# Kernel optimization log

Measured on AMD Instinct MI355X. Metric: run time of the kernel, lower is better.

Reference implementation:

```python
import jax, jax.numpy as jnp
import numpy as np

B, N, D, H, M, O = 8, 1024, 256, 512, 256, 256


def _mlp(x, W1, b1, W2, b2):
    # two-layer MLP: Linear -> ReLU -> Linear (torch Linear: x @ W.T + b)
    return jax.nn.relu(x @ W1.T + b1) @ W2.T + b2


def _lstm(x, W_ih, W_hh, b):
    # x: [B, N, D] -> h: [B, N, H]; single-layer unidirectional LSTM, torch gate order i,f,g,o
    Bt, Nt, _ = x.shape
    x_proj = x @ W_ih.T + b  # [B, N, 4H] precompute input projection

    def step(carry, xt):
        h, c = carry
        gates = xt + h @ W_hh.T
        i, f, g, o = jnp.split(gates, 4, axis=-1)
        i, f, o = jax.nn.sigmoid(i), jax.nn.sigmoid(f), jax.nn.sigmoid(o)
        c = f * c + i * jnp.tanh(g)
        h = o * jnp.tanh(c)
        return (h, c), h

    h0 = jnp.zeros((Bt, W_hh.shape[1]), x.dtype)
    (_, _), hs = jax.lax.scan(step, (h0, h0), jnp.swapaxes(x_proj, 0, 1))
    return jnp.swapaxes(hs, 0, 1)


def setup_inputs() -> dict:
    key = jax.random.key(0)
    ks = jax.random.split(key, 32)
    p = lambda k, s: jax.random.normal(k, s, jnp.float32) * 0.02
    inp = {
        "feats": jax.random.normal(ks[0], (B, N, D), jnp.float32),
        "adj": jax.random.randint(ks[1], (B, N, N), 0, 2, jnp.int32),
        "W_ih": p(ks[2], (4 * H, D)),
        "W_hh": p(ks[3], (4 * H, H)),
        "b_ih": jnp.zeros((4 * H,), jnp.float32),
        "b_hh": jnp.zeros((4 * H,), jnp.float32),
        "gx_W1": p(ks[4], (M, H)), "gx_b1": jnp.zeros((M,), jnp.float32),
        "gx_W2": p(ks[5], (M, M)), "gx_b2": jnp.zeros((M,), jnp.float32),
        "gz_W1": p(ks[6], (M, H)), "gz_b1": jnp.zeros((M,), jnp.float32),
        "gz_W2": p(ks[7], (M, M)), "gz_b2": jnp.zeros((M,), jnp.float32),
        "gv_W1": p(ks[8], (M, H)), "gv_b1": jnp.zeros((M,), jnp.float32),
        "gv_W2": p(ks[9], (M, M)), "gv_b2": jnp.zeros((M,), jnp.float32),
        "gn_W1": p(ks[10], (M, M)), "gn_b1": jnp.zeros((M,), jnp.float32),
        "gn_W2": p(ks[11], (O, M)), "gn_b2": jnp.zeros((O,), jnp.float32),
        "out_W": p(ks[12], (O, H + O)), "out_b": jnp.zeros((O,), jnp.float32),
    }
    return inp


def reference(feats, adj, W_ih, W_hh, b_ih, b_hh,
              gx_W1, gx_b1, gx_W2, gx_b2,
              gz_W1, gz_b1, gz_W2, gz_b2,
              gv_W1, gv_b1, gv_W2, gv_b2,
              gn_W1, gn_b1, gn_W2, gn_b2,
              out_W, out_b):
    h = _lstm(feats, W_ih, W_hh, b_ih + b_hh)  # [B, N, H]

    # Note: in the source, concat_1[:, :lstm_hidden_dim] == s_i and
    # concat_2[:, :lstm_hidden_dim] == s_j, so scores = <g_x(s_i), g_v(s_j)>
    ax = _mlp(h, gx_W1, gx_b1, gx_W2, gx_b2)  # [B, N, M]
    av = _mlp(h, gv_W1, gv_b1, gv_W2, gv_b2)  # [B, N, M]
    scores = jnp.einsum('bim,bjm->bij', ax, av)  # [B, N, N]

    eye = jnp.eye(N, dtype=bool)
    mask = (adj > 0) & ~eye[None]  # valid neighbors
    w = jax.nn.softmax(jnp.where(mask, scores, -1e30), axis=-1)
    w = w * mask  # zero out rows with no neighbors (softmax of all -inf -> uniform)

    sagg = jnp.einsum('bij,bjh->bih', w, h)  # weighted neighbor sum [B, N, H]
    agg = _mlp(_mlp(sagg, gz_W1, gz_b1, gz_W2, gz_b2), gn_W1, gn_b1, gn_W2, gn_b2)
    has_nb = mask.any(axis=-1, keepdims=True)  # [B, N, 1]
    agg = jnp.where(has_nb, agg, 0.0)  # isolated nodes get zero aggregate

    combined = jnp.concatenate([h, agg], axis=-1)  # [B, N, H+O]
    return combined @ out_W.T + out_b
```

## Files before the change

### kernel.cpp

```cpp
#include <hip/hip_runtime.h>

typedef unsigned short u16;
typedef unsigned long long u64;
using short8 = __attribute__((ext_vector_type(8))) short;
using f32x4  = __attribute__((ext_vector_type(4))) float;

#define GF_RELU  1
#define GF_F32   2
#define GF_XPOSE 4

__device__ __forceinline__ float b2f(u16 x) {
    unsigned u = ((unsigned)x) << 16;
    return __builtin_bit_cast(float, u);
}
__device__ __forceinline__ u16 f2b(float f) {
    unsigned u = __builtin_bit_cast(unsigned, f);
    unsigned r = u + 0x7FFFu + ((u >> 16) & 1u);
    return (u16)(r >> 16);
}
__device__ __forceinline__ f32x4 mfma_bf16(uint4 a, uint4 b, f32x4 c) {
    return __builtin_amdgcn_mfma_f32_16x16x32_bf16(
        __builtin_bit_cast(short8, a), __builtin_bit_cast(short8, b), c, 0, 0, 0);
}
__device__ __forceinline__ f32x4 zero4() { f32x4 z = {0.f, 0.f, 0.f, 0.f}; return z; }

__global__ __launch_bounds__(256) void cvt_bf16(const float* __restrict__ src,
                                                u16* __restrict__ dst, int n) {
    for (int i = blockIdx.x * 256 + threadIdx.x; i < n; i += gridDim.x * 256)
        dst[i] = f2b(src[i]);
}

__global__ void pack_params(const float* __restrict__ Whh, const float* __restrict__ Wih,
                            const float* __restrict__ bih, const float* __restrict__ bhh,
                            u16* __restrict__ WhhP, u16* __restrict__ WihP,
                            float* __restrict__ biasP) {
    int p = blockIdx.x;
    int t = threadIdx.x;
    int orig = ((p & 3) << 9) + (p >> 2);
    WhhP[((long)p << 9) + t]       = f2b(Whh[((long)orig << 9) + t]);
    WhhP[((long)p << 9) + 256 + t] = f2b(Whh[((long)orig << 9) + 256 + t]);
    WihP[((long)p << 8) + t]       = f2b(Wih[((long)orig << 8) + t]);
    if (t == 0) biasP[p] = bih[orig] + bhh[orig];
}

__global__ __launch_bounds__(256) void gemm_bt(
    const u16* __restrict__ A, const u16* __restrict__ A2, int ksplit,
    const u16* __restrict__ B, void* __restrict__ Cout,
    int M, int N, int K,
    long sAb, long sBb, long sCb,
    const float* __restrict__ bias, const float* __restrict__ rowmask, int flags) {
    __shared__ __align__(16) u16 As[64][40];
    __shared__ __align__(16) u16 Bs[128][40];
    const int bz = blockIdx.z;
    const u16* Ab = A + (long)bz * sAb;
    const u16* Bb = B + (long)bz * sBb;
    const int m0 = blockIdx.x << 6, n0 = blockIdx.y << 7;
    const int tid = threadIdx.x;
    const int lane = tid & 63, wave = tid >> 6;
    const int srow = tid >> 2, skc = (tid & 3) << 3;
    const int frm = lane & 15, fq = lane >> 4;

    auto loadA = [&](int ka) -> uint4 {
        const u16* p = (ka < ksplit)
            ? Ab + (long)(m0 + srow) * ksplit + ka
            : A2 + (long)(m0 + srow) * (K - ksplit) + (ka - ksplit);
        return *(const uint4*)p;
    };
    const u16* Brow0 = Bb + (long)(n0 + srow) * K;
    const u16* Brow1 = Bb + (long)(n0 + 64 + srow) * K;

    f32x4 acc[8];
#pragma unroll
    for (int i = 0; i < 8; i++) acc[i] = zero4();

    uint4 a  = loadA(skc);
    uint4 b0 = *(const uint4*)(Brow0 + skc);
    uint4 b1 = *(const uint4*)(Brow1 + skc);

    for (int k0 = 0; k0 < K; k0 += 32) {
        __syncthreads();
        *(uint4*)&As[srow][skc] = a;
        *(uint4*)&Bs[srow][skc] = b0;
        *(uint4*)&Bs[64 + srow][skc] = b1;
        __syncthreads();
        int kn = k0 + 32;
        if (kn < K) {
            a  = loadA(kn + skc);
            b0 = *(const uint4*)(Brow0 + kn + skc);
            b1 = *(const uint4*)(Brow1 + kn + skc);
        }
        uint4 af = *(const uint4*)&As[(wave << 4) + frm][fq << 3];
#pragma unroll
        for (int nt = 0; nt < 8; nt++) {
            uint4 bf = *(const uint4*)&Bs[(nt << 4) + frm][fq << 3];
            acc[nt] = mfma_bf16(af, bf, acc[nt]);
        }
    }
#pragma unroll
    for (int nt = 0; nt < 8; nt++) {
        int col = n0 + (nt << 4) + frm;
        float bv = bias ? bias[col] : 0.f;
#pragma unroll
        for (int r = 0; r < 4; r++) {
            int row = m0 + (wave << 4) + (fq << 2) + r;
            float v = acc[nt][r] + bv;
            if (flags & GF_RELU) v = fmaxf(v, 0.f);
            if (rowmask) v *= rowmask[row];
            long orow = (flags & GF_XPOSE) ? (long)((row & 1023) * 8 + (row >> 10))
                                           : (long)row;
            if (flags & GF_F32)
                ((float*)Cout)[(long)bz * sCb + orow * N + col] = v;
            else
                ((u16*)Cout)[(long)bz * sCb + orow * N + col] = f2b(v);
        }
    }
}

template<bool L2C>
__device__ __forceinline__ void lstm_loop(
    const u16* __restrict__ xproj, u16* __restrict__ h, u64* __restrict__ hx,
    const uint4 (&bfrag)[2][16], unsigned* hsh, int* hflag,
    int g, int s, int wv, int lane, int frm, int fq, int colbase) {
    float creg = 0.f;
    int budget = 1 << 20;

#pragma unroll 1
    for (int t = 0; t < 1024; t++) {
        float xp0 = b2f(xproj[((long)(t * 8 + g) << 11) + colbase + frm]);
        float xp1 = b2f(xproj[((long)(t * 8 + g) << 11) + colbase + 16 + frm]);

        float s0, s1;
        if (t > 0) {
            if (wv == 0) {
                const u64* buf = hx + (g << 9) + (((t - 1) & 1) << 8);
                const u64* p0 = buf + lane;
                const u64* p1 = buf + 64 + lane;
                const u64* p2 = buf + 128 + lane;
                const u64* p3 = buf + 192 + lane;
                u64 v0, v1, v2, v3;
                const unsigned want = (unsigned)t;
                while (true) {
                    if constexpr (L2C) {
                        u64 z = 0;
                        asm volatile(
                            "global_atomic_add_x2 %0, %4, %8, off sc0\n\t"
                            "global_atomic_add_x2 %1, %5, %8, off sc0\n\t"
                            "global_atomic_add_x2 %2, %6, %8, off sc0\n\t"
                            "global_atomic_add_x2 %3, %7, %8, off sc0\n\t"
                            "s_waitcnt vmcnt(0)"
                            : "=&v"(v0), "=&v"(v1), "=&v"(v2), "=&v"(v3)
                            : "v"(p0), "v"(p1), "v"(p2), "v"(p3), "v"(z)
                            : "memory");
                    } else {
                        asm volatile(
                            "global_load_dwordx2 %0, %4, off sc0 sc1\n\t"
                            "global_load_dwordx2 %1, %5, off sc0 sc1\n\t"
                            "global_load_dwordx2 %2, %6, off sc0 sc1\n\t"
                            "global_load_dwordx2 %3, %7, off sc0 sc1\n\t"
                            "s_waitcnt vmcnt(0)"
                            : "=&v"(v0), "=&v"(v1), "=&v"(v2), "=&v"(v3)
                            : "v"(p0), "v"(p1), "v"(p2), "v"(p3)
                            : "memory");
                    }
                    bool ok = ((unsigned)(v0 >> 32) == want) &
                              ((unsigned)(v1 >> 32) == want) &
                              ((unsigned)(v2 >> 32) == want) &
                              ((unsigned)(v3 >> 32) == want);
                    if (__all(ok) || --budget < 0) break;
                }
                hsh[lane]       = (unsigned)v0;
                hsh[64 + lane]  = (unsigned)v1;
                hsh[128 + lane] = (unsigned)v2;
                hsh[192 + lane] = (unsigned)v3;
                __threadfence_block();
                if (lane == 0)
                    __hip_atomic_store(hflag, t, __ATOMIC_RELAXED,
                                       __HIP_MEMORY_SCOPE_WORKGROUP);
            } else {
                while (__hip_atomic_load(hflag, __ATOMIC_RELAXED,
                                         __HIP_MEMORY_SCOPE_WORKGROUP) < t) {
                    if (--budget < 0) break;
                }
                __threadfence_block();
            }

            f32x4 a0p[4], a1p[4];
#pragma unroll
            for (int r = 0; r < 4; r++) { a0p[r] = zero4(); a1p[r] = zero4(); }
#pragma unroll
            for (int r4 = 0; r4 < 4; r4++) {
                uint4 af[4];
#pragma unroll
                for (int q = 0; q < 4; q++)
                    af[q] = *(const uint4*)&hsh[(((r4 << 2) | q) << 4) + (fq << 2)];
#pragma unroll
                for (int q = 0; q < 4; q++) {
                    a0p[r4] = mfma_bf16(af[q], bfrag[0][(r4 << 2) | q], a0p[r4]);
                    a1p[r4] = mfma_bf16(af[q], bfrag[1][(r4 << 2) | q], a1p[r4]);
                }
            }
            s0 = (a0p[0][0] + a0p[1][0]) + (a0p[2][0] + a0p[3][0]) + xp0;
            s1 = (a1p[0][0] + a1p[1][0]) + (a1p[2][0] + a1p[3][0]) + xp1;
        } else {
            s0 = xp0;
            s1 = xp1;
        }

        float ss[4];
#pragma unroll
        for (int k = 0; k < 4; k++) {
            int src = ((lane << 2) + k) & 15;
            float t0 = __shfl(s0, src);
            float t1 = __shfl(s1, src);
            ss[k] = (lane < 4) ? t0 : t1;
        }
        float iv = 1.f / (1.f + __expf(-ss[0]));
        float fv = 1.f / (1.f + __expf(-ss[1]));
        float gv = 1.f - 2.f / (__expf(2.f * ss[2]) + 1.f);
        float ov = 1.f / (1.f + __expf(-ss[3]));
        creg = fv * creg + iv * gv;
        float hv = ov * (1.f - 2.f / (__expf(2.f * creg) + 1.f));
        float hn = __shfl_down(hv, 1);
        if (lane < 8 && !(lane & 1)) {
            unsigned dw = (unsigned)f2b(hv) | ((unsigned)f2b(hn) << 16);
            int d = (s << 5) + (wv << 2) + (lane >> 1);
            u64 pv = ((u64)(unsigned)(t + 1) << 32) | (u64)dw;
            u64* dst = &hx[(g << 9) + ((t & 1) << 8) + d];
            if constexpr (L2C) {
                asm volatile("global_atomic_swap_x2 %0, %1, off"
                             :: "v"(dst), "v"(pv) : "memory");
            } else {
                asm volatile("global_store_dwordx2 %0, %1, off sc0 sc1"
                             :: "v"(dst), "v"(pv) : "memory");
            }
            ((unsigned*)h)[(((long)(g * 1024 + t)) << 8) + d] = dw;
        }
    }
}

__global__ __launch_bounds__(512, 1) void lstm_rec(
    const u16* __restrict__ WhhP, const u16* __restrict__ xproj,
    u16* __restrict__ h, u64* __restrict__ hx, unsigned* __restrict__ xcdid) {
    __shared__ __align__(16) unsigned hshare[256];
    __shared__ int hflag;
    const int bid = blockIdx.x;
    const int g = bid & 7;
    const int s = bid >> 3;
    const int tid = threadIdx.x;
    const int lane = tid & 63, wv = tid >> 6;
    const int frm = lane & 15, fq = lane >> 4;
    const int colbase = (s << 8) + (wv << 5);

    uint4 bfrag[2][16];
#pragma unroll
    for (int T = 0; T < 2; T++)
#pragma unroll
        for (int kk = 0; kk < 16; kk++)
            bfrag[T][kk] = *(const uint4*)&WhhP[((long)(colbase + (T << 4) + frm) << 9) +
                                                (kk << 5) + (fq << 3)];

    unsigned myxcd;
    asm volatile("s_getreg_b32 %0, hwreg(HW_REG_XCC_ID)" : "=s"(myxcd));
    if (tid == 0) {
        hflag = -1;
        unsigned val = 0x100u | (myxcd & 0xffu);
        asm volatile("global_store_dword %0, %1, off sc0 sc1"
                     :: "v"(&xcdid[bid]), "v"(val) : "memory");
    }
    const unsigned* pid = &xcdid[g + ((lane & 7) << 3)];
    unsigned idv = 0;
    int bd = 1 << 22;
    while (true) {
        asm volatile("global_load_dword %0, %1, off sc0 sc1\n\ts_waitcnt vmcnt(0)"
                     : "=&v"(idv) : "v"(pid) : "memory");
        if (__all((idv >> 8) == 1u) || --bd < 0) break;
    }
    bool same = (bd >= 0) && __all((idv & 0xffu) == (__shfl(idv, 0) & 0xffu));
    __syncthreads();

    if (same)
        lstm_loop<true>(xproj, h, hx, bfrag, hshare, &hflag,
                        g, s, wv, lane, frm, fq, colbase);
    else
        lstm_loop<false>(xproj, h, hx, bfrag, hshare, &hflag,
                         g, s, wv, lane, frm, fq, colbase);
}

__global__ __launch_bounds__(256) void transpose_h(const u16* __restrict__ h,
                                                   u16* __restrict__ hT) {
    __shared__ __align__(16) u16 tile[64][72];
    const int b = blockIdx.z;
    const int t0 = blockIdx.x << 6, u0 = blockIdx.y << 6;
    const int tid = threadIdx.x;
    const int r = tid >> 3, c8 = (tid & 7) << 3;
#pragma unroll
    for (int j = 0; j < 2; j++) {
        int row = r + (j << 5);
        *(uint4*)&tile[row][c8] =
            *(const uint4*)&h[(((long)b << 10) + t0 + row) * 512 + u0 + c8];
    }
    __syncthreads();
#pragma unroll
    for (int j = 0; j < 2; j++) {
        int urow = r + (j << 5);
        unsigned wds[4];
#pragma unroll
        for (int k = 0; k < 4; k++) {
            unsigned lo = tile[c8 + (k << 1)][urow];
            unsigned hi = tile[c8 + (k << 1) + 1][urow];
            wds[k] = lo | (hi << 16);
        }
        uint4 v; v.x = wds[0]; v.y = wds[1]; v.z = wds[2]; v.w = wds[3];
        *(uint4*)&hT[(((long)b << 9) + u0 + urow) * 1024 + t0 + c8] = v;
    }
}

__global__ __launch_bounds__(256) void softmax_row(
    const float* __restrict__ scores, const int* __restrict__ adj,
    u16* __restrict__ w, float* __restrict__ hasnb) {
    __shared__ float red[4];
    const int row = blockIdx.x;
    const int i = row & 1023;
    const int tid = threadIdx.x;
    const int lane = tid & 63, wave = tid >> 6;
    const float* s = scores + ((long)row << 10);
    const int* arow = adj + ((long)row << 10);

    float sv[4]; bool mk[4];
    float mx = -3.0e38f;
#pragma unroll
    for (int q = 0; q < 4; q++) {
        int j = tid + (q << 8);
        mk[q] = (arow[j] > 0) && (j != i);
        sv[q] = s[j];
        if (mk[q]) mx = fmaxf(mx, sv[q]);
    }
    for (int off = 32; off; off >>= 1) mx = fmaxf(mx, __shfl_xor(mx, off));
    if (lane == 0) red[wave] = mx;
    __syncthreads();
    mx = fmaxf(fmaxf(red[0], red[1]), fmaxf(red[2], red[3]));
    float e[4]; float sum = 0.f;
#pragma unroll
    for (int q = 0; q < 4; q++) {
        e[q] = mk[q] ? __expf(sv[q] - mx) : 0.f;
        sum += e[q];
    }
    __syncthreads();
    for (int off = 32; off; off >>= 1) sum += __shfl_xor(sum, off);
    if (lane == 0) red[wave] = sum;
    __syncthreads();
    sum = red[0] + red[1] + red[2] + red[3];
    float inv = sum > 0.f ? 1.f / sum : 0.f;
#pragma unroll
    for (int q = 0; q < 4; q++) {
        int j = tid + (q << 8);
        w[((long)row << 10) + j] = f2b(e[q] * inv);
    }
    if (tid == 0) hasnb[row] = sum > 0.f ? 1.f : 0.f;
}

extern "C" void kernel_launch(void* const* d_in, const int* in_sizes, int n_in,
                              void* d_out, int out_size, void* d_ws, size_t ws_size,
                              hipStream_t stream) {
    const float* feats = (const float*)d_in[0];
    const int*   adj   = (const int*)d_in[1];
    const float* W_ih  = (const float*)d_in[2];
    const float* W_hh  = (const float*)d_in[3];
    const float* b_ih  = (const float*)d_in[4];
    const float* b_hh  = (const float*)d_in[5];
    const float* gx_W1 = (const float*)d_in[6];  const float* gx_b1 = (const float*)d_in[7];
    const float* gx_W2 = (const float*)d_in[8];  const float* gx_b2 = (const float*)d_in[9];
    const float* gz_W1 = (const float*)d_in[10]; const float* gz_b1 = (const float*)d_in[11];
    const float* gz_W2 = (const float*)d_in[12]; const float* gz_b2 = (const float*)d_in[13];
    const float* gv_W1 = (const float*)d_in[14]; const float* gv_b1 = (const float*)d_in[15];
    const float* gv_W2 = (const float*)d_in[16]; const float* gv_b2 = (const float*)d_in[17];
    const float* gn_W1 = (const float*)d_in[18]; const float* gn_b1 = (const float*)d_in[19];
    const float* gn_W2 = (const float*)d_in[20]; const float* gn_b2 = (const float*)d_in[21];
    const float* out_W = (const float*)d_in[22]; const float* out_b = (const float*)d_in[23];

    char* ws = (char*)d_ws;
    size_t off = 0;
    auto alloc = [&](size_t bytes) {
        void* p = ws + off;
        off += (bytes + 255) & ~(size_t)255;
        return p;
    };
    u16* WhhP      = (u16*)alloc(2048L * 512 * 2);
    u16* WihP      = (u16*)alloc(2048L * 256 * 2);
    float* biasP   = (float*)alloc(2048L * 4);
    u64* hx        = (u64*)alloc(8L * 512 * 8);
    unsigned* xcdid = (unsigned*)alloc(64L * 4);
    u16* featsB    = (u16*)alloc(8192L * 256 * 2);
    u16* gxW1b     = (u16*)alloc(256L * 512 * 2);
    u16* gxW2b     = (u16*)alloc(256L * 256 * 2);
    u16* gvW1b     = (u16*)alloc(256L * 512 * 2);
    u16* gvW2b     = (u16*)alloc(256L * 256 * 2);
    u16* gzW1b     = (u16*)alloc(256L * 512 * 2);
    u16* gzW2b     = (u16*)alloc(256L * 256 * 2);
    u16* gnW1b     = (u16*)alloc(256L * 256 * 2);
    u16* gnW2b     = (u16*)alloc(256L * 256 * 2);
    u16* outWb     = (u16*)alloc(256L * 768 * 2);
    u16* xproj     = (u16*)alloc(8L * 1024 * 2048 * 2);
    u16* h         = (u16*)alloc(8L * 1024 * 512 * 2);
    u16* hT        = (u16*)alloc(8L * 1024 * 512 * 2);
    u16* t1        = (u16*)alloc(8192L * 256 * 2);
    u16* tB        = (u16*)alloc(8192L * 256 * 2);
    u16* ax        = (u16*)alloc(8192L * 256 * 2);
    u16* av        = (u16*)alloc(8192L * 256 * 2);
    u16* agg       = (u16*)alloc(8192L * 256 * 2);
    float* hasnb   = (float*)alloc(8192L * 4);
    float* scores  = (float*)alloc(8L * 1024 * 1024 * 4);
    u16* w         = (u16*)alloc(8L * 1024 * 1024 * 2);
    if (off > ws_size) return;

    hipMemsetAsync(hx, 0, 8L * 512 * 8, stream);
    hipMemsetAsync(xcdid, 0, 64L * 4, stream);
    pack_params<<<2048, 256, 0, stream>>>(W_hh, W_ih, b_ih, b_hh, WhhP, WihP, biasP);

    auto cvt = [&](const float* src, u16* dst, int n) {
        cvt_bf16<<<(n + 1023) / 1024, 256, 0, stream>>>(src, dst, n);
    };
    cvt(feats, featsB, 8192 * 256);
    cvt(gx_W1, gxW1b, 256 * 512);  cvt(gx_W2, gxW2b, 256 * 256);
    cvt(gv_W1, gvW1b, 256 * 512);  cvt(gv_W2, gvW2b, 256 * 256);
    cvt(gz_W1, gzW1b, 256 * 512);  cvt(gz_W2, gzW2b, 256 * 256);
    cvt(gn_W1, gnW1b, 256 * 256);  cvt(gn_W2, gnW2b, 256 * 256);
    cvt(out_W, outWb, 256 * 768);

    gemm_bt<<<dim3(128, 16, 1), 256, 0, stream>>>(
        featsB, nullptr, 256, WihP, xproj, 8192, 2048, 256, 0, 0, 0,
        biasP, nullptr, GF_XPOSE);

    lstm_rec<<<64, 512, 0, stream>>>(WhhP, xproj, h, hx, xcdid);

    transpose_h<<<dim3(16, 8, 8), 256, 0, stream>>>(h, hT);

    gemm_bt<<<dim3(128, 2, 1), 256, 0, stream>>>(
        h, nullptr, 512, gxW1b, t1, 8192, 256, 512, 0, 0, 0, gx_b1, nullptr, GF_RELU);
    gemm_bt<<<dim3(128, 2, 1), 256, 0, stream>>>(
        t1, nullptr, 256, gxW2b, ax, 8192, 256, 256, 0, 0, 0, gx_b2, nullptr, 0);
    gemm_bt<<<dim3(128, 2, 1), 256, 0, stream>>>(
        h, nullptr, 512, gvW1b, t1, 8192, 256, 512, 0, 0, 0, gv_b1, nullptr, GF_RELU);
    gemm_bt<<<dim3(128, 2, 1), 256, 0, stream>>>(
        t1, nullptr, 256, gvW2b, av, 8192, 256, 256, 0, 0, 0, gv_b2, nullptr, 0);

    gemm_bt<<<dim3(16, 8, 8), 256, 0, stream>>>(
        ax, nullptr, 256, av, scores, 1024, 1024, 256,
        262144, 262144, 1048576, nullptr, nullptr, GF_F32);

    softmax_row<<<8192, 256, 0, stream>>>(scores, adj, w, hasnb);

    u16* sagg = xproj;
    gemm_bt<<<dim3(16, 4, 8), 256, 0, stream>>>(
        w, nullptr, 1024, hT, sagg, 1024, 512, 1024,
        1048576, 524288, 524288, nullptr, nullptr, 0);

    gemm_bt<<<dim3(128, 2, 1), 256, 0, stream>>>(
        sagg, nullptr, 512, gzW1b, t1, 8192, 256, 512, 0, 0, 0, gz_b1, nullptr, GF_RELU);
    gemm_bt<<<dim3(128, 2, 1), 256, 0, stream>>>(
        t1, nullptr, 256, gzW2b, tB, 8192, 256, 256, 0, 0, 0, gz_b2, nullptr, 0);
    gemm_bt<<<dim3(128, 2, 1), 256, 0, stream>>>(
        tB, nullptr, 256, gnW1b, t1, 8192, 256, 256, 0, 0, 0, gn_b1, nullptr, GF_RELU);
    gemm_bt<<<dim3(128, 2, 1), 256, 0, stream>>>(
        t1, nullptr, 256, gnW2b, agg, 8192, 256, 256, 0, 0, 0, gn_b2, hasnb, 0);

    gemm_bt<<<dim3(128, 2, 1), 256, 0, stream>>>(
        h, agg, 512, outWb, (float*)d_out, 8192, 256, 768, 0, 0, 0, out_b, nullptr, GF_F32);
}
```

Before: 2.422 ms.

## Replace double-buffered hidden-state exchange with per-step ring and scalar tag polling

The LSTM recurrence exchanged hidden states between blocks through a two-slot buffer polled with L2 atomics. It now writes each timestep into its own slot of a full-length ring, which reuses the scores and w scratch buffers. Each block publishes a per-step tag after a block barrier, and same-XCD consumers poll those tags with scalar loads after a dcache invalidate, then read the data with plain loads. This is meant to cut the cost of per-step atomic polling, in exchange for an extra __syncthreads per step, duplicated stores, and reliance on cache-coherence assumptions about plain stores and scalar loads.

```diff
diff --git a/kernel.cpp b/kernel.cpp
--- a/kernel.cpp
+++ b/kernel.cpp
@@ -4,6 +4,7 @@
 typedef unsigned long long u64;
 using short8 = __attribute__((ext_vector_type(8))) short;
 using f32x4  = __attribute__((ext_vector_type(4))) float;
+using u32x8  = __attribute__((ext_vector_type(8))) unsigned;
 
 #define GF_RELU  1
 #define GF_F32   2
@@ -118,9 +119,10 @@
 
 template<bool L2C>
 __device__ __forceinline__ void lstm_loop(
-    const u16* __restrict__ xproj, u16* __restrict__ h, u64* __restrict__ hx,
+    const u16* __restrict__ xproj, u16* __restrict__ h,
+    u64* __restrict__ ring, unsigned* __restrict__ tags,
     const uint4 (&bfrag)[2][16], unsigned* hsh, int* hflag,
-    int g, int s, int wv, int lane, int frm, int fq, int colbase) {
+    int g, int s, int wv, int lane, int frm, int fq, int colbase, int tid) {
     float creg = 0.f;
     int budget = 1 << 20;
 
@@ -131,27 +133,46 @@
 
         float s0, s1;
         if (t > 0) {
+            const unsigned want = (unsigned)t;
+            const u64* slot = ring + (((long)((g << 10) + (t - 1))) << 8);
             if (wv == 0) {
-                const u64* buf = hx + (g << 9) + (((t - 1) & 1) << 8);
-                const u64* p0 = buf + lane;
-                const u64* p1 = buf + 64 + lane;
-                const u64* p2 = buf + 128 + lane;
-                const u64* p3 = buf + 192 + lane;
+                if constexpr (L2C) {
+                    const unsigned* tbase = tags + (((g << 10) + (t - 1)) << 3);
+                    u64 ta = (u64)tbase;
+                    unsigned tlo = __builtin_amdgcn_readfirstlane((unsigned)ta);
+                    unsigned thi = __builtin_amdgcn_readfirstlane((unsigned)(ta >> 32));
+                    u64 tsg = ((u64)thi << 32) | tlo;
+                    while (true) {
+                        u32x8 tg;
+                        asm volatile(
+                            "s_dcache_inv\n\t"
+                            "s_waitcnt lgkmcnt(0)\n\t"
+                            "s_load_dwordx8 %0, %1, 0\n\t"
+                            "s_waitcnt lgkmcnt(0)"
+                            : "=s"(tg) : "s"(tsg) : "memory");
+                        bool ok = (tg[0] == want) & (tg[1] == want) &
+                                  (tg[2] == want) & (tg[3] == want) &
+                                  (tg[4] == want) & (tg[5] == want) &
+                                  (tg[6] == want) & (tg[7] == want);
+                        if (ok || --budget < 0) break;
+                    }
+                }
+                const u64* p0 = slot + lane;
+                const u64* p1 = slot + 64 + lane;
+                const u64* p2 = slot + 128 + lane;
+                const u64* p3 = slot + 192 + lane;
                 u64 v0, v1, v2, v3;
-                const unsigned want = (unsigned)t;
-                while (true) {
-                    if constexpr (L2C) {
-                        u64 z = 0;
-                        asm volatile(
-                            "global_atomic_add_x2 %0, %4, %8, off sc0\n\t"
-                            "global_atomic_add_x2 %1, %5, %8, off sc0\n\t"
-                            "global_atomic_add_x2 %2, %6, %8, off sc0\n\t"
-                            "global_atomic_add_x2 %3, %7, %8, off sc0\n\t"
-                            "s_waitcnt vmcnt(0)"
-                            : "=&v"(v0), "=&v"(v1), "=&v"(v2), "=&v"(v3)
-                            : "v"(p0), "v"(p1), "v"(p2), "v"(p3), "v"(z)
-                            : "memory");
-                    } else {
+                bool need_mall = true;
+                if constexpr (L2C) {
+                    v0 = p0[0]; v1 = p1[0]; v2 = p2[0]; v3 = p3[0];
+                    bool ok = ((unsigned)(v0 >> 32) == want) &
+                              ((unsigned)(v1 >> 32) == want) &
+                              ((unsigned)(v2 >> 32) == want) &
+                              ((unsigned)(v3 >> 32) == want);
+                    need_mall = !__all(ok);
+                }
+                if (need_mall) {
+                    while (true) {
                         asm volatile(
                             "global_load_dwordx2 %0, %4, off sc0 sc1\n\t"
                             "global_load_dwordx2 %1, %5, off sc0 sc1\n\t"
@@ -161,12 +182,12 @@
                             : "=&v"(v0), "=&v"(v1), "=&v"(v2), "=&v"(v3)
                             : "v"(p0), "v"(p1), "v"(p2), "v"(p3)
                             : "memory");
+                        bool ok = ((unsigned)(v0 >> 32) == want) &
+                                  ((unsigned)(v1 >> 32) == want) &
+                                  ((unsigned)(v2 >> 32) == want) &
+                                  ((unsigned)(v3 >> 32) == want);
+                        if (__all(ok) || --budget < 0) break;
                     }
-                    bool ok = ((unsigned)(v0 >> 32) == want) &
-                              ((unsigned)(v1 >> 32) == want) &
-                              ((unsigned)(v2 >> 32) == want) &
-                              ((unsigned)(v3 >> 32) == want);
-                    if (__all(ok) || --budget < 0) break;
                 }
                 hsh[lane]       = (unsigned)v0;
                 hsh[64 + lane]  = (unsigned)v1;
@@ -221,26 +242,37 @@
         creg = fv * creg + iv * gv;
         float hv = ov * (1.f - 2.f / (__expf(2.f * creg) + 1.f));
         float hn = __shfl_down(hv, 1);
-        if (lane < 8 && !(lane & 1)) {
+
+        const bool pub = (lane < 8) && !(lane & 1);
+        u64 pv = 0; u64* dst = nullptr;
+        if (pub) {
             unsigned dw = (unsigned)f2b(hv) | ((unsigned)f2b(hn) << 16);
             int d = (s << 5) + (wv << 2) + (lane >> 1);
-            u64 pv = ((u64)(unsigned)(t + 1) << 32) | (u64)dw;
-            u64* dst = &hx[(g << 9) + ((t & 1) << 8) + d];
+            pv = ((u64)(unsigned)(t + 1) << 32) | (u64)dw;
+            dst = ring + (((long)((g << 10) + t)) << 8) + d;
             if constexpr (L2C) {
-                asm volatile("global_atomic_swap_x2 %0, %1, off"
-                             :: "v"(dst), "v"(pv) : "memory");
+                *dst = pv;
             } else {
                 asm volatile("global_store_dwordx2 %0, %1, off sc0 sc1"
                              :: "v"(dst), "v"(pv) : "memory");
             }
             ((unsigned*)h)[(((long)(g * 1024 + t)) << 8) + d] = dw;
         }
+        if constexpr (L2C) {
+            __syncthreads();
+            if (tid == 0)
+                tags[(((g << 10) + t) << 3) + s] = (unsigned)(t + 1);
+            if (pub)
+                asm volatile("global_store_dwordx2 %0, %1, off sc0 sc1"
+                             :: "v"(dst), "v"(pv) : "memory");
+        }
     }
 }
 
 __global__ __launch_bounds__(512, 1) void lstm_rec(
     const u16* __restrict__ WhhP, const u16* __restrict__ xproj,
-    u16* __restrict__ h, u64* __restrict__ hx, unsigned* __restrict__ xcdid) {
+    u16* __restrict__ h, u64* __restrict__ ring, unsigned* __restrict__ tags,
+    unsigned* __restrict__ xcdid) {
     __shared__ __align__(16) unsigned hshare[256];
     __shared__ int hflag;
     const int bid = blockIdx.x;
@@ -279,11 +311,11 @@
     __syncthreads();
 
     if (same)
-        lstm_loop<true>(xproj, h, hx, bfrag, hshare, &hflag,
-                        g, s, wv, lane, frm, fq, colbase);
+        lstm_loop<true>(xproj, h, ring, tags, bfrag, hshare, &hflag,
+                        g, s, wv, lane, frm, fq, colbase, tid);
     else
-        lstm_loop<false>(xproj, h, hx, bfrag, hshare, &hflag,
-                         g, s, wv, lane, frm, fq, colbase);
+        lstm_loop<false>(xproj, h, ring, tags, bfrag, hshare, &hflag,
+                         g, s, wv, lane, frm, fq, colbase, tid);
 }
 
 __global__ __launch_bounds__(256) void transpose_h(const u16* __restrict__ h,
@@ -388,7 +420,6 @@
     u16* WhhP      = (u16*)alloc(2048L * 512 * 2);
     u16* WihP      = (u16*)alloc(2048L * 256 * 2);
     float* biasP   = (float*)alloc(2048L * 4);
-    u64* hx        = (u64*)alloc(8L * 512 * 8);
     unsigned* xcdid = (unsigned*)alloc(64L * 4);
     u16* featsB    = (u16*)alloc(8192L * 256 * 2);
     u16* gxW1b     = (u16*)alloc(256L * 512 * 2);
@@ -413,8 +444,11 @@
     u16* w         = (u16*)alloc(8L * 1024 * 1024 * 2);
     if (off > ws_size) return;
 
-    hipMemsetAsync(hx, 0, 8L * 512 * 8, stream);
-    hipMemsetAsync(xcdid, 0, 64L * 4, stream);
+    u64* ring      = (u64*)w;
+    unsigned* tags = (unsigned*)scores;
+
+    (void)hipMemsetAsync(tags, 0, 8L * 1024 * 8 * 4, stream);
+    (void)hipMemsetAsync(xcdid, 0, 64L * 4, stream);
     pack_params<<<2048, 256, 0, stream>>>(W_hh, W_ih, b_ih, b_hh, WhhP, WihP, biasP);
 
     auto cvt = [&](const float* src, u16* dst, int n) {
@@ -431,7 +465,7 @@
         featsB, nullptr, 256, WihP, xproj, 8192, 2048, 256, 0, 0, 0,
         biasP, nullptr, GF_XPOSE);
 
-    lstm_rec<<<64, 512, 0, stream>>>(WhhP, xproj, h, hx, xcdid);
+    lstm_rec<<<64, 512, 0, stream>>>(WhhP, xproj, h, ring, tags, xcdid);
 
     transpose_h<<<dim3(16, 8, 8), 256, 0, stream>>>(h, hT);
 
```

After: 2.458 ms. Within noise of the previous version (+1.5%).
